# Kernel tuning notes

Hardware: AMD Instinct MI355X
Metric: run time of the kernel (lower is better)

## Reference

```python
import jax, jax.numpy as jnp
import numpy as np

N_NODES = 100000
N_EDGES = 3200000
IN_DIM = 512
HID_DIM = 16
OUT_DIM = 64


def _gcn_layer(E, X, W, b, n_nodes):
    # Standard GCN layer (CatGNN GCNLayer_MPNN_2):
    # add self-loops, symmetric deg^-1/2 normalization, project, gather-scatter sum.
    src = jnp.concatenate([E[0], jnp.arange(n_nodes, dtype=E.dtype)])
    dst = jnp.concatenate([E[1], jnp.arange(n_nodes, dtype=E.dtype)])
    deg = jax.ops.segment_sum(jnp.ones_like(dst, dtype=X.dtype), dst, num_segments=n_nodes)
    dinv = jnp.where(deg > 0, jax.lax.rsqrt(deg), 0.0)  # deg^-1/2, safe
    h = X @ W  # [N, d_out] project BEFORE aggregation (cheaper gather)
    norm = dinv[src] * dinv[dst]  # [E+N]
    msg = h[src] * norm[:, None]  # gather + scale
    out = jax.ops.segment_sum(msg, dst, num_segments=n_nodes)  # scatter-sum
    return out + b


def setup_inputs() -> dict:
    key = jax.random.key(0)
    k1, k2, k3, k4, k5 = jax.random.split(key, 5)
    V = jnp.arange(N_NODES, dtype=jnp.int64)
    E = jax.random.randint(k1, (2, N_EDGES), 0, N_NODES, dtype=jnp.int64)
    X = jax.random.normal(k2, (N_NODES, IN_DIM), dtype=jnp.float32)
    # Glorot-style init for layer weights
    W1 = jax.random.normal(k3, (IN_DIM, HID_DIM), dtype=jnp.float32) / np.sqrt(IN_DIM)
    b1 = jnp.zeros((HID_DIM,), dtype=jnp.float32)
    W2 = jax.random.normal(k4, (HID_DIM, OUT_DIM), dtype=jnp.float32) / np.sqrt(HID_DIM)
    b2 = jnp.zeros((OUT_DIM,), dtype=jnp.float32)
    return {"V": V, "E": E, "X": X, "W1": W1, "b1": b1, "W2": W2, "b2": b2}


def reference(V, E, X, W1, b1, W2, b2):
    n_nodes = V.shape[0]
    H = jax.nn.relu(_gcn_layer(E, X, W1, b1, n_nodes))
    # dropout is identity in eval mode
    H = _gcn_layer(E, H, W2, b2, n_nodes)
    return H
```

## Files before the change

kernel.cpp:

```cpp
#include <hip/hip_runtime.h>

#define HID 16
#define ODIM 64
#define IDIM 512
#define BKB 8
#define BKS 256
#define PTILE 4096
#define MAXBE 12288

__global__ __launch_bounds__(256) void k_bhist(const int* __restrict__ dst,
                                               int* __restrict__ bcnt, int ne, int nbk) {
    __shared__ int h[512];
    for (int t = threadIdx.x; t < 512; t += 256) h[t] = 0;
    __syncthreads();
    int stride = gridDim.x * blockDim.x;
    for (int e = blockIdx.x * blockDim.x + threadIdx.x; e < ne; e += stride)
        atomicAdd(&h[dst[e] >> BKB], 1);
    __syncthreads();
    for (int t = threadIdx.x; t < nbk; t += 256)
        if (h[t]) atomicAdd(&bcnt[t], h[t]);
}

__global__ __launch_bounds__(512) void k_bscan(const int* __restrict__ bcnt,
                                               int* __restrict__ bbase,
                                               int* __restrict__ bcur, int nbk) {
    __shared__ int s[512];
    int t = threadIdx.x;
    int v = (t < nbk) ? bcnt[t] : 0;
    s[t] = v;
    __syncthreads();
    for (int off = 1; off < 512; off <<= 1) {
        int u = (t >= off) ? s[t - off] : 0;
        __syncthreads();
        s[t] += u;
        __syncthreads();
    }
    if (t < nbk) { int b = s[t] - v; bbase[t] = b; bcur[t] = b; }
}

__global__ __launch_bounds__(512) void k_part(const int* __restrict__ src,
                                              const int* __restrict__ dst,
                                              int* __restrict__ bcur,
                                              unsigned int* __restrict__ ebuf,
                                              int ne, int nbk) {
    __shared__ int h[512], sc[512], base[512], lcur[512];
    __shared__ unsigned int sval[PTILE];
    __shared__ int saddr[PTILE];
    int e0 = blockIdx.x * PTILE;
    int m = ne - e0; if (m > PTILE) m = PTILE;
    if (m <= 0) return;
    int t = threadIdx.x;
    h[t] = 0;
    __syncthreads();
    for (int k = t; k < m; k += 512) atomicAdd(&h[dst[e0 + k] >> BKB], 1);
    __syncthreads();
    int hv = h[t];
    sc[t] = hv;
    __syncthreads();
    for (int off = 1; off < 512; off <<= 1) {
        int u = (t >= off) ? sc[t - off] : 0;
        __syncthreads();
        sc[t] += u;
        __syncthreads();
    }
    base[t] = hv ? atomicAdd(&bcur[t], hv) : 0;
    lcur[t] = 0;
    __syncthreads();
    for (int k = t; k < m; k += 512) {
        int d = dst[e0 + k];
        int b = d >> BKB;
        int r = atomicAdd(&lcur[b], 1);
        int slot = sc[b] - h[b] + r;
        sval[slot] = ((unsigned int)src[e0 + k] << BKB) | (unsigned int)(d & (BKS - 1));
        saddr[slot] = base[b] + r;
    }
    __syncthreads();
    for (int k = t; k < m; k += 512) ebuf[saddr[k]] = sval[k];
}

__global__ __launch_bounds__(256) void k_csr(const int* __restrict__ bbase,
                                             const int* __restrict__ bcnt,
                                             const unsigned int* __restrict__ ebuf,
                                             int* __restrict__ cnt,
                                             int* __restrict__ row_start,
                                             int* __restrict__ csr_src, int n) {
    __shared__ int h[256], sc[256], lc[256];
    __shared__ int stage[MAXBE];
    int bk = blockIdx.x;
    int node0 = bk << BKB;
    int ebase = bbase[bk];
    int ecnt = bcnt[bk];
    int t = threadIdx.x;
    h[t] = 0; lc[t] = 0;
    __syncthreads();
    for (int k = t; k < ecnt; k += 256) atomicAdd(&h[ebuf[ebase + k] & (BKS - 1)], 1);
    __syncthreads();
    int hv = h[t];
    sc[t] = hv;
    __syncthreads();
    for (int off = 1; off < 256; off <<= 1) {
        int u = (t >= off) ? sc[t - off] : 0;
        __syncthreads();
        sc[t] += u;
        __syncthreads();
    }
    int node = node0 + t;
    if (node < n) { cnt[node] = hv; row_start[node] = ebase + sc[t] - hv; }
    if (ecnt <= MAXBE) {
        for (int k = t; k < ecnt; k += 256) {
            unsigned int p = ebuf[ebase + k];
            int dl = p & (BKS - 1);
            int r = atomicAdd(&lc[dl], 1);
            stage[sc[dl] - h[dl] + r] = (int)(p >> BKB);
        }
        __syncthreads();
        for (int k = t; k < ecnt; k += 256) csr_src[ebase + k] = stage[k];
    } else {
        for (int k = t; k < ecnt; k += 256) {
            unsigned int p = ebuf[ebase + k];
            int dl = p & (BKS - 1);
            int r = atomicAdd(&lc[dl], 1);
            csr_src[ebase + sc[dl] - h[dl] + r] = (int)(p >> BKB);
        }
    }
}

__global__ __launch_bounds__(256) void k_proj1(const float* __restrict__ X,
                                               const float* __restrict__ W1,
                                               const int* __restrict__ cnt,
                                               float* __restrict__ hs1, int n) {
    __shared__ float Ws[IDIM * HID];
    for (int t = threadIdx.x; t < IDIM * HID; t += 256) Ws[t] = W1[t];
    __syncthreads();

    int i = blockIdx.x * blockDim.x + threadIdx.x;
    if (i >= n) return;

    const float4* xr = (const float4*)(X + (size_t)i * IDIM);
    float acc[HID];
#pragma unroll
    for (int j = 0; j < HID; ++j) acc[j] = 0.f;

    for (int k4 = 0; k4 < IDIM / 4; ++k4) {
        float4 x = xr[k4];
        const float* w = &Ws[k4 * 4 * HID];
#pragma unroll
        for (int j = 0; j < HID; ++j) acc[j] += x.x * w[j];
#pragma unroll
        for (int j = 0; j < HID; ++j) acc[j] += x.y * w[HID + j];
#pragma unroll
        for (int j = 0; j < HID; ++j) acc[j] += x.z * w[2 * HID + j];
#pragma unroll
        for (int j = 0; j < HID; ++j) acc[j] += x.w * w[3 * HID + j];
    }

    float di = rsqrtf((float)(cnt[i] + 1));
    float4* h4 = (float4*)(hs1 + (size_t)i * HID);
#pragma unroll
    for (int q = 0; q < 4; ++q) {
        float4 v;
        v.x = acc[q * 4 + 0] * di;
        v.y = acc[q * 4 + 1] * di;
        v.z = acc[q * 4 + 2] * di;
        v.w = acc[q * 4 + 3] * di;
        h4[q] = v;
    }
}

__global__ __launch_bounds__(256) void k_gather(const int* __restrict__ row_start,
                                                const int* __restrict__ cnt,
                                                const int* __restrict__ csr_src,
                                                const float* __restrict__ hs,
                                                float* __restrict__ agg, int n) {
    int tid = blockIdx.x * blockDim.x + threadIdx.x;
    int i = tid >> 2;
    int q = tid & 3;
    if (i >= n) return;
    int rs = row_start[i];
    int c = cnt[i];
    const float4* h4 = (const float4*)hs;
    float4 acc = h4[(size_t)i * 4 + q];
    int k = 0;
    for (; k + 1 < c; k += 2) {
        int s0 = csr_src[rs + k];
        int s1 = csr_src[rs + k + 1];
        float4 v0 = h4[(size_t)s0 * 4 + q];
        float4 v1 = h4[(size_t)s1 * 4 + q];
        acc.x += v0.x; acc.y += v0.y; acc.z += v0.z; acc.w += v0.w;
        acc.x += v1.x; acc.y += v1.y; acc.z += v1.z; acc.w += v1.w;
    }
    if (k < c) {
        int s0 = csr_src[rs + k];
        float4 v0 = h4[(size_t)s0 * 4 + q];
        acc.x += v0.x; acc.y += v0.y; acc.z += v0.z; acc.w += v0.w;
    }
    ((float4*)agg)[(size_t)i * 4 + q] = acc;
}

__global__ void k_mid(const int* __restrict__ cnt, const float* __restrict__ b1,
                      float* __restrict__ buf, int n) {
    int t = blockIdx.x * blockDim.x + threadIdx.x;
    if (t >= n * HID) return;
    int i = t >> 4;
    int j = t & 15;
    float di = rsqrtf((float)(cnt[i] + 1));
    float h = di * buf[t] + b1[j];
    h = fmaxf(h, 0.f);
    buf[t] = h * di;
}

__global__ __launch_bounds__(256) void k_out(const int* __restrict__ cnt,
                                             const float* __restrict__ agg2,
                                             const float* __restrict__ W2,
                                             const float* __restrict__ b2,
                                             float* __restrict__ out, int n) {
    __shared__ float Ws[HID * ODIM];
    __shared__ float bs[ODIM];
    for (int t = threadIdx.x; t < HID * ODIM; t += 256) Ws[t] = W2[t];
    if (threadIdx.x < ODIM) bs[threadIdx.x] = b2[threadIdx.x];
    __syncthreads();

    int t = blockIdx.x * blockDim.x + threadIdx.x;
    if (t >= n * ODIM) return;
    int i = t >> 6;
    int j = t & 63;
    float di = rsqrtf((float)(cnt[i] + 1));
    const float* g = agg2 + (size_t)i * HID;
    float acc = 0.f;
#pragma unroll
    for (int k = 0; k < HID; ++k) acc += g[k] * Ws[k * ODIM + j];
    out[t] = di * acc + bs[j];
}

extern "C" void kernel_launch(void* const* d_in, const int* in_sizes, int n_in,
                              void* d_out, int out_size, void* d_ws, size_t ws_size,
                              hipStream_t stream) {
    const int* E = (const int*)d_in[1];
    const float* X = (const float*)d_in[2];
    const float* W1 = (const float*)d_in[3];
    const float* b1 = (const float*)d_in[4];
    const float* W2 = (const float*)d_in[5];
    const float* b2 = (const float*)d_in[6];
    float* out = (float*)d_out;

    const int n = in_sizes[0];
    const int ne = in_sizes[1] / 2;
    const int* src = E;
    const int* dst = E + ne;
    const int nbk = (n + BKS - 1) >> BKB;

    char* ws = (char*)d_ws;
    int* bcnt = (int*)ws;
    int* bbase = (int*)(ws + (8u << 10));
    int* bcur = (int*)(ws + (16u << 10));
    int* cnt = (int*)(ws + (1u << 20));
    int* row_start = (int*)(ws + (2u << 20));
    unsigned int* ebuf = (unsigned int*)(ws + (3u << 20));
    float* B1 = (float*)(ws + (3u << 20));
    float* B2 = (float*)(ws + (10u << 20));
    int* csr_src = (int*)(ws + (17u << 20));

    hipMemsetAsync(bcnt, 0, nbk * sizeof(int), stream);
    k_bhist<<<1024, 256, 0, stream>>>(dst, bcnt, ne, nbk);
    k_bscan<<<1, 512, 0, stream>>>(bcnt, bbase, bcur, nbk);
    k_part<<<(ne + PTILE - 1) / PTILE, 512, 0, stream>>>(src, dst, bcur, ebuf, ne, nbk);
    k_csr<<<nbk, 256, 0, stream>>>(bbase, bcnt, ebuf, cnt, row_start, csr_src, n);

    k_proj1<<<(n + 255) / 256, 256, 0, stream>>>(X, W1, cnt, B1, n);
    k_gather<<<(n * 4 + 255) / 256, 256, 0, stream>>>(row_start, cnt, csr_src, B1, B2, n);
    k_mid<<<(n * HID + 255) / 256, 256, 0, stream>>>(cnt, b1, B2, n);
    k_gather<<<(n * 4 + 255) / 256, 256, 0, stream>>>(row_start, cnt, csr_src, B2, B1, n);
    k_out<<<(n * ODIM + 255) / 256, 256, 0, stream>>>(cnt, B1, W2, b2, out, n);
}
```

Baseline: 588.6 us.

## Fuse mid activation into gather, vectorize gather indices, rework proj1/out/csr kernels

Folds the bias+ReLU+rescale step into the first gather kernel, removing one launch and a full read/write pass over the hidden buffer. The gather now loads four CSR indices at a time with an aligned int4 read after a short head loop. k_proj1 drops the shared-memory copy of W1 and reads weights as float4 straight from global memory with explicit FMAs. k_out caches a W2 column in registers and handles four nodes per thread. k_csr moves to 512 threads per block. Reading W1 from global instead of LDS depends on cache behaviour, and the extra csr threads sit idle during the 256-wide scan.

```diff
diff --git a/kernel.cpp b/kernel.cpp
--- a/kernel.cpp
+++ b/kernel.cpp
@@ -78,7 +78,7 @@
     for (int k = t; k < m; k += 512) ebuf[saddr[k]] = sval[k];
 }
 
-__global__ __launch_bounds__(256) void k_csr(const int* __restrict__ bbase,
+__global__ __launch_bounds__(512) void k_csr(const int* __restrict__ bbase,
                                              const int* __restrict__ bcnt,
                                              const unsigned int* __restrict__ ebuf,
                                              int* __restrict__ cnt,
@@ -91,32 +91,34 @@
     int ebase = bbase[bk];
     int ecnt = bcnt[bk];
     int t = threadIdx.x;
-    h[t] = 0; lc[t] = 0;
-    __syncthreads();
-    for (int k = t; k < ecnt; k += 256) atomicAdd(&h[ebuf[ebase + k] & (BKS - 1)], 1);
-    __syncthreads();
-    int hv = h[t];
-    sc[t] = hv;
+    if (t < 256) { h[t] = 0; lc[t] = 0; }
+    __syncthreads();
+    for (int k = t; k < ecnt; k += 512) atomicAdd(&h[ebuf[ebase + k] & (BKS - 1)], 1);
+    __syncthreads();
+    int hv = (t < 256) ? h[t] : 0;
+    if (t < 256) sc[t] = hv;
     __syncthreads();
     for (int off = 1; off < 256; off <<= 1) {
-        int u = (t >= off) ? sc[t - off] : 0;
-        __syncthreads();
-        sc[t] += u;
-        __syncthreads();
-    }
-    int node = node0 + t;
-    if (node < n) { cnt[node] = hv; row_start[node] = ebase + sc[t] - hv; }
+        int u = (t >= off && t < 256) ? sc[t - off] : 0;
+        __syncthreads();
+        if (t < 256) sc[t] += u;
+        __syncthreads();
+    }
+    if (t < 256) {
+        int node = node0 + t;
+        if (node < n) { cnt[node] = hv; row_start[node] = ebase + sc[t] - hv; }
+    }
     if (ecnt <= MAXBE) {
-        for (int k = t; k < ecnt; k += 256) {
+        for (int k = t; k < ecnt; k += 512) {
             unsigned int p = ebuf[ebase + k];
             int dl = p & (BKS - 1);
             int r = atomicAdd(&lc[dl], 1);
             stage[sc[dl] - h[dl] + r] = (int)(p >> BKB);
         }
         __syncthreads();
-        for (int k = t; k < ecnt; k += 256) csr_src[ebase + k] = stage[k];
+        for (int k = t; k < ecnt; k += 512) csr_src[ebase + k] = stage[k];
     } else {
-        for (int k = t; k < ecnt; k += 256) {
+        for (int k = t; k < ecnt; k += 512) {
             unsigned int p = ebuf[ebase + k];
             int dl = p & (BKS - 1);
             int r = atomicAdd(&lc[dl], 1);
@@ -125,46 +127,93 @@
     }
 }
 
+__device__ __forceinline__ void fmaq(float4& a, float s, float4 w) {
+    a.x = fmaf(s, w.x, a.x);
+    a.y = fmaf(s, w.y, a.y);
+    a.z = fmaf(s, w.z, a.z);
+    a.w = fmaf(s, w.w, a.w);
+}
+
 __global__ __launch_bounds__(256) void k_proj1(const float* __restrict__ X,
                                                const float* __restrict__ W1,
                                                const int* __restrict__ cnt,
                                                float* __restrict__ hs1, int n) {
-    __shared__ float Ws[IDIM * HID];
-    for (int t = threadIdx.x; t < IDIM * HID; t += 256) Ws[t] = W1[t];
-    __syncthreads();
-
-    int i = blockIdx.x * blockDim.x + threadIdx.x;
+    int i = blockIdx.x * 256 + threadIdx.x;
     if (i >= n) return;
 
-    const float4* xr = (const float4*)(X + (size_t)i * IDIM);
-    float acc[HID];
-#pragma unroll
-    for (int j = 0; j < HID; ++j) acc[j] = 0.f;
+    const float4* __restrict__ xr = (const float4*)(X + (size_t)i * IDIM);
+    const float4* __restrict__ W4 = (const float4*)W1;
+    float4 a0 = make_float4(0.f, 0.f, 0.f, 0.f), a1 = a0, a2 = a0, a3 = a0;
 
     for (int k4 = 0; k4 < IDIM / 4; ++k4) {
         float4 x = xr[k4];
-        const float* w = &Ws[k4 * 4 * HID];
-#pragma unroll
-        for (int j = 0; j < HID; ++j) acc[j] += x.x * w[j];
-#pragma unroll
-        for (int j = 0; j < HID; ++j) acc[j] += x.y * w[HID + j];
-#pragma unroll
-        for (int j = 0; j < HID; ++j) acc[j] += x.z * w[2 * HID + j];
-#pragma unroll
-        for (int j = 0; j < HID; ++j) acc[j] += x.w * w[3 * HID + j];
+        const float4* w = W4 + k4 * 16;
+        fmaq(a0, x.x, w[0]);  fmaq(a1, x.x, w[1]);  fmaq(a2, x.x, w[2]);  fmaq(a3, x.x, w[3]);
+        fmaq(a0, x.y, w[4]);  fmaq(a1, x.y, w[5]);  fmaq(a2, x.y, w[6]);  fmaq(a3, x.y, w[7]);
+        fmaq(a0, x.z, w[8]);  fmaq(a1, x.z, w[9]);  fmaq(a2, x.z, w[10]); fmaq(a3, x.z, w[11]);
+        fmaq(a0, x.w, w[12]); fmaq(a1, x.w, w[13]); fmaq(a2, x.w, w[14]); fmaq(a3, x.w, w[15]);
     }
 
     float di = rsqrtf((float)(cnt[i] + 1));
+    a0.x *= di; a0.y *= di; a0.z *= di; a0.w *= di;
+    a1.x *= di; a1.y *= di; a1.z *= di; a1.w *= di;
+    a2.x *= di; a2.y *= di; a2.z *= di; a2.w *= di;
+    a3.x *= di; a3.y *= di; a3.z *= di; a3.w *= di;
     float4* h4 = (float4*)(hs1 + (size_t)i * HID);
-#pragma unroll
-    for (int q = 0; q < 4; ++q) {
-        float4 v;
-        v.x = acc[q * 4 + 0] * di;
-        v.y = acc[q * 4 + 1] * di;
-        v.z = acc[q * 4 + 2] * di;
-        v.w = acc[q * 4 + 3] * di;
-        h4[q] = v;
-    }
+    h4[0] = a0; h4[1] = a1; h4[2] = a2; h4[3] = a3;
+}
+
+__device__ __forceinline__ float4 gacc(int rs, int c, int q,
+                                       const int* __restrict__ csr_src,
+                                       const float4* __restrict__ h4,
+                                       float4 acc) {
+    int k = 0;
+    int head = (-rs) & 3;
+    if (head > c) head = c;
+    for (; k < head; ++k) {
+        float4 v = h4[(size_t)csr_src[rs + k] * 4 + q];
+        acc.x += v.x; acc.y += v.y; acc.z += v.z; acc.w += v.w;
+    }
+    for (; k + 3 < c; k += 4) {
+        int4 s = *(const int4*)(csr_src + rs + k);
+        float4 v0 = h4[(size_t)s.x * 4 + q];
+        float4 v1 = h4[(size_t)s.y * 4 + q];
+        float4 v2 = h4[(size_t)s.z * 4 + q];
+        float4 v3 = h4[(size_t)s.w * 4 + q];
+        acc.x += v0.x; acc.y += v0.y; acc.z += v0.z; acc.w += v0.w;
+        acc.x += v1.x; acc.y += v1.y; acc.z += v1.z; acc.w += v1.w;
+        acc.x += v2.x; acc.y += v2.y; acc.z += v2.z; acc.w += v2.w;
+        acc.x += v3.x; acc.y += v3.y; acc.z += v3.z; acc.w += v3.w;
+    }
+    for (; k < c; ++k) {
+        float4 v = h4[(size_t)csr_src[rs + k] * 4 + q];
+        acc.x += v.x; acc.y += v.y; acc.z += v.z; acc.w += v.w;
+    }
+    return acc;
+}
+
+__global__ __launch_bounds__(256) void k_gather_mid(const int* __restrict__ row_start,
+                                                    const int* __restrict__ cnt,
+                                                    const int* __restrict__ csr_src,
+                                                    const float* __restrict__ hs,
+                                                    const float* __restrict__ b1,
+                                                    float* __restrict__ outbuf, int n) {
+    int tid = blockIdx.x * blockDim.x + threadIdx.x;
+    int i = tid >> 2;
+    int q = tid & 3;
+    if (i >= n) return;
+    const float4* h4 = (const float4*)hs;
+    int rs = row_start[i];
+    int c = cnt[i];
+    float4 acc = gacc(rs, c, q, csr_src, h4, h4[(size_t)i * 4 + q]);
+    float di = rsqrtf((float)(c + 1));
+    float4 b = ((const float4*)b1)[q];
+    float4 r;
+    r.x = fmaxf(fmaf(di, acc.x, b.x), 0.f) * di;
+    r.y = fmaxf(fmaf(di, acc.y, b.y), 0.f) * di;
+    r.z = fmaxf(fmaf(di, acc.z, b.z), 0.f) * di;
+    r.w = fmaxf(fmaf(di, acc.w, b.w), 0.f) * di;
+    ((float4*)outbuf)[(size_t)i * 4 + q] = r;
 }
 
 __global__ __launch_bounds__(256) void k_gather(const int* __restrict__ row_start,
@@ -176,37 +225,11 @@
     int i = tid >> 2;
     int q = tid & 3;
     if (i >= n) return;
+    const float4* h4 = (const float4*)hs;
     int rs = row_start[i];
     int c = cnt[i];
-    const float4* h4 = (const float4*)hs;
-    float4 acc = h4[(size_t)i * 4 + q];
-    int k = 0;
-    for (; k + 1 < c; k += 2) {
-        int s0 = csr_src[rs + k];
-        int s1 = csr_src[rs + k + 1];
-        float4 v0 = h4[(size_t)s0 * 4 + q];
-        float4 v1 = h4[(size_t)s1 * 4 + q];
-        acc.x += v0.x; acc.y += v0.y; acc.z += v0.z; acc.w += v0.w;
-        acc.x += v1.x; acc.y += v1.y; acc.z += v1.z; acc.w += v1.w;
-    }
-    if (k < c) {
-        int s0 = csr_src[rs + k];
-        float4 v0 = h4[(size_t)s0 * 4 + q];
-        acc.x += v0.x; acc.y += v0.y; acc.z += v0.z; acc.w += v0.w;
-    }
+    float4 acc = gacc(rs, c, q, csr_src, h4, h4[(size_t)i * 4 + q]);
     ((float4*)agg)[(size_t)i * 4 + q] = acc;
-}
-
-__global__ void k_mid(const int* __restrict__ cnt, const float* __restrict__ b1,
-                      float* __restrict__ buf, int n) {
-    int t = blockIdx.x * blockDim.x + threadIdx.x;
-    if (t >= n * HID) return;
-    int i = t >> 4;
-    int j = t & 15;
-    float di = rsqrtf((float)(cnt[i] + 1));
-    float h = di * buf[t] + b1[j];
-    h = fmaxf(h, 0.f);
-    buf[t] = h * di;
 }
 
 __global__ __launch_bounds__(256) void k_out(const int* __restrict__ cnt,
@@ -216,20 +239,37 @@
                                              float* __restrict__ out, int n) {
     __shared__ float Ws[HID * ODIM];
     __shared__ float bs[ODIM];
-    for (int t = threadIdx.x; t < HID * ODIM; t += 256) Ws[t] = W2[t];
-    if (threadIdx.x < ODIM) bs[threadIdx.x] = b2[threadIdx.x];
-    __syncthreads();
-
-    int t = blockIdx.x * blockDim.x + threadIdx.x;
-    if (t >= n * ODIM) return;
-    int i = t >> 6;
+    int t = threadIdx.x;
+    for (int u = t; u < HID * ODIM; u += 256) Ws[u] = W2[u];
+    if (t < ODIM) bs[t] = b2[t];
+    __syncthreads();
+
     int j = t & 63;
-    float di = rsqrtf((float)(cnt[i] + 1));
-    const float* g = agg2 + (size_t)i * HID;
-    float acc = 0.f;
+    int slot = t >> 6;
+    int i0 = blockIdx.x * 16 + slot * 4;
+
+    float wc[HID];
 #pragma unroll
-    for (int k = 0; k < HID; ++k) acc += g[k] * Ws[k * ODIM + j];
-    out[t] = di * acc + bs[j];
+    for (int k = 0; k < HID; ++k) wc[k] = Ws[k * ODIM + j];
+    float bj = bs[j];
+
+    const float4* g4 = (const float4*)agg2;
+#pragma unroll
+    for (int u = 0; u < 4; ++u) {
+        int i = i0 + u;
+        if (i < n) {
+            float4 g0 = g4[(size_t)i * 4 + 0];
+            float4 g1 = g4[(size_t)i * 4 + 1];
+            float4 g2 = g4[(size_t)i * 4 + 2];
+            float4 g3 = g4[(size_t)i * 4 + 3];
+            float acc = g0.x * wc[0]  + g0.y * wc[1]  + g0.z * wc[2]  + g0.w * wc[3]
+                      + g1.x * wc[4]  + g1.y * wc[5]  + g1.z * wc[6]  + g1.w * wc[7]
+                      + g2.x * wc[8]  + g2.y * wc[9]  + g2.z * wc[10] + g2.w * wc[11]
+                      + g3.x * wc[12] + g3.y * wc[13] + g3.z * wc[14] + g3.w * wc[15];
+            float di = rsqrtf((float)(cnt[i] + 1));
+            out[(size_t)i * ODIM + j] = fmaf(di, acc, bj);
+        }
+    }
 }
 
 extern "C" void kernel_launch(void* const* d_in, const int* in_sizes, int n_in,
@@ -264,11 +304,10 @@
     k_bhist<<<1024, 256, 0, stream>>>(dst, bcnt, ne, nbk);
     k_bscan<<<1, 512, 0, stream>>>(bcnt, bbase, bcur, nbk);
     k_part<<<(ne + PTILE - 1) / PTILE, 512, 0, stream>>>(src, dst, bcur, ebuf, ne, nbk);
-    k_csr<<<nbk, 256, 0, stream>>>(bbase, bcnt, ebuf, cnt, row_start, csr_src, n);
+    k_csr<<<nbk, 512, 0, stream>>>(bbase, bcnt, ebuf, cnt, row_start, csr_src, n);
 
     k_proj1<<<(n + 255) / 256, 256, 0, stream>>>(X, W1, cnt, B1, n);
-    k_gather<<<(n * 4 + 255) / 256, 256, 0, stream>>>(row_start, cnt, csr_src, B1, B2, n);
-    k_mid<<<(n * HID + 255) / 256, 256, 0, stream>>>(cnt, b1, B2, n);
+    k_gather_mid<<<(n * 4 + 255) / 256, 256, 0, stream>>>(row_start, cnt, csr_src, B1, b1, B2, n);
     k_gather<<<(n * 4 + 255) / 256, 256, 0, stream>>>(row_start, cnt, csr_src, B2, B1, n);
-    k_out<<<(n * ODIM + 255) / 256, 256, 0, stream>>>(cnt, B1, W2, b2, out, n);
-}
+    k_out<<<(n + 15) / 16, 256, 0, stream>>>(cnt, B1, W2, b2, out, n);
+}
```

After: 528.4 us. -10.2%, faster.
